# Performance work log

Hardware: AMD Instinct MI355X
Metric: run time of the kernel (lower is better)

The kernel has to match this reference:

```python
import jax, jax.numpy as jnp
import numpy as np

D_MODEL = 1024
N_HEADS = 16
D_K = D_MODEL // N_HEADS
THETA = 10000.0
B, S = 4, 2048


def setup_inputs() -> dict:
    key = jax.random.key(0)
    ks = jax.random.split(key, 5)
    scale = 0.02
    return {
        "x": jax.random.normal(ks[0], (B, S, D_MODEL), dtype=jnp.float32),
        "token_positions": jnp.arange(S, dtype=jnp.int32),
        "WQ": jax.random.normal(ks[1], (D_MODEL, D_MODEL), dtype=jnp.float32) * scale,
        "WK": jax.random.normal(ks[2], (D_MODEL, D_MODEL), dtype=jnp.float32) * scale,
        "WV": jax.random.normal(ks[3], (D_MODEL, D_MODEL), dtype=jnp.float32) * scale,
        "WO": jax.random.normal(ks[4], (D_MODEL, D_MODEL), dtype=jnp.float32) * scale,
    }


def apply_rope(x, positions):
    # x: [B, H, S, d_k]; rotate interleaved (even, odd) pairs
    half = D_K // 2
    inv_freq = THETA ** (-jnp.arange(half, dtype=x.dtype) * 2.0 / D_K)  # [half]
    ang = positions.astype(x.dtype)[:, None] * inv_freq[None, :]        # [S, half]
    cos, sin = jnp.cos(ang), jnp.sin(ang)
    x1 = x[..., 0::2]
    x2 = x[..., 1::2]
    r1 = x1 * cos - x2 * sin
    r2 = x1 * sin + x2 * cos
    return jnp.stack([r1, r2], axis=-1).reshape(x.shape)


def reference(x, token_positions, WQ, WK, WV, WO):
    b, s, _ = x.shape
    # Linear (no bias), weight stored (out, in): y = x @ W^T
    def proj(W):
        y = jnp.einsum('bsd,ed->bse', x, W)
        return y.reshape(b, s, N_HEADS, D_K).transpose(0, 2, 1, 3)  # [b,h,s,dk]
    Q, K, V = proj(WQ), proj(WK), proj(WV)
    Q = apply_rope(Q, token_positions)
    K = apply_rope(K, token_positions)
    scores = jnp.einsum('bhqd,bhkd->bhqk', Q, K) / jnp.sqrt(jnp.asarray(D_K, x.dtype))
    causal = jnp.tril(jnp.ones((s, s), dtype=bool))
    scores = jnp.where(causal, scores, -jnp.inf)
    attn = jax.nn.softmax(scores, axis=-1)
    out = jnp.einsum('bhqk,bhkd->bhqd', attn, V)
    out = out.transpose(0, 2, 1, 3).reshape(b, s, D_MODEL)
    return jnp.einsum('bse,de->bsd', out, WO)
```

## Files before the change

### kernel.cpp

```cpp
#include <hip/hip_runtime.h>
#include <cstdint>
#include <cstddef>

#define DM 1024
#define NH 16
#define DKD 64
#define BB 4
#define SS 2048
#define MTOT (BB*SS)

typedef float  f32x4  __attribute__((ext_vector_type(4)));
typedef __bf16 bf16x8 __attribute__((ext_vector_type(8)));
typedef __bf16 bf16x4v __attribute__((ext_vector_type(4)));
typedef __bf16 bf16x2v __attribute__((ext_vector_type(2)));
using as3v = __attribute__((address_space(3))) void;
using as1v = __attribute__((address_space(1))) void;

__device__ __forceinline__ void gl2lds16(const void* g, void* l) {
  __builtin_amdgcn_global_load_lds((as1v*)g, (as3v*)l, 16, 0, 0);
}

__device__ __forceinline__ float fast_exp2(float x) {
#if __has_builtin(__builtin_amdgcn_exp2f)
  return __builtin_amdgcn_exp2f(x);
#else
  return __expf(x * 0.6931471805599453f);
#endif
}

__device__ __forceinline__ void sincos_rev(float rev, float* s, float* c) {
#if __has_builtin(__builtin_amdgcn_sinf) && __has_builtin(__builtin_amdgcn_cosf)
  *s = __builtin_amdgcn_sinf(rev);
  *c = __builtin_amdgcn_cosf(rev);
#else
  float a = rev * 6.283185307179586f;
  *s = __sinf(a); *c = __cosf(a);
#endif
}

__device__ __forceinline__ uint32_t pkbf(float a, float b) {
  union { uint32_t u; __bf16 h[2]; } c;
  c.h[0] = (__bf16)a; c.h[1] = (__bf16)b;
  return c.u;
}

__global__ void cast_all_k(const float* __restrict__ x,
                           const float* __restrict__ wq, const float* __restrict__ wk,
                           const float* __restrict__ wv, const float* __restrict__ wo,
                           __bf16* __restrict__ xb,
                           __bf16* __restrict__ wqb, __bf16* __restrict__ wkb,
                           __bf16* __restrict__ wvb, __bf16* __restrict__ wob) {
  int i = blockIdx.x * blockDim.x + threadIdx.x;
  const float* src;
  __bf16* dst;
  int idx, oidx;
  if (i < 2097152) {
    src = x; dst = xb; idx = i; oidx = i;
  } else {
    int j = i - 2097152;
    int w = j >> 18;
    idx = j & 262143;
    src = (w == 0) ? wq : (w == 1) ? wk : (w == 2) ? wv : wo;
    dst = (w == 0) ? wqb : (w == 1) ? wkb : (w == 2) ? wvb : wob;
    if (w < 2) {
      int e = idx >> 8;
      int c = idx & 255;
      int d = e & 63;
      int dp = (d & 1) ? 32 + (d >> 1) : (d >> 1);
      oidx = (((e & ~63) | dp) << 8) | c;
    } else {
      oidx = idx;
    }
  }
  float4 f = ((const float4*)src)[idx];
  bf16x4v o;
  o[0] = (__bf16)f.x; o[1] = (__bf16)f.y; o[2] = (__bf16)f.z; o[3] = (__bf16)f.w;
  ((bf16x4v*)dst)[oidx] = o;
}

__global__ void rope_tbl_k(const int* __restrict__ pos, float2* __restrict__ tbl) {
  int p = blockIdx.x * blockDim.x + threadIdx.x;
  int s = p >> 5;
  int i = p & 31;
  float ps = (float)pos[s];
  float invr = __expf(-0.28782313663f * (float)i) * 0.15915494309f;
  float rev = ps * invr;
  rev -= floorf(rev);
  float sn, cs;
  sincos_rev(rev, &sn, &cs);
  tbl[p] = make_float2(cs, sn);
}


template <typename CT>
__global__ __launch_bounds__(256, 4) void gemm_bt_k(const __bf16* __restrict__ A,
                                                    const __bf16* __restrict__ B,
                                                    CT* __restrict__ C,
                                                    int M, int N, int K) {
  __shared__ __bf16 As[2][128 * 32];
  __shared__ __bf16 Bs[2][128 * 32];
  const int tid  = threadIdx.x;
  const int lane = tid & 63;
  const int wid  = tid >> 6;
  const int lrow = lane & 15;
  const int quad = lane >> 4;
  const int m0 = blockIdx.y * 128;
  const int n0 = blockIdx.x * 128;
  const int wm = (wid & 1) * 64;
  const int wn = (wid >> 1) * 64;

  const int r0 = wid * 32 + (lane >> 2);
  const int cs = (((r0 & 1) << 2) | (lane & 3)) ^ ((r0 >> 1) & 7);
  const int gr = (r0 & ~1) | (cs >> 2);
  const int gc = cs & 3;
  const __bf16* Asrc = A + (size_t)(m0 + gr) * K + gc * 8;
  const __bf16* Bsrc = B + (size_t)(n0 + gr) * K + gc * 8;
  const int clf = (((lrow & 1) << 2) + quad) ^ (lrow >> 1);

  f32x4 acc[4][4] = {};

  auto stage = [&](int buf, int k0) {
    gl2lds16(Asrc + k0,                   &As[buf][(wid * 32)      * 32]);
    gl2lds16(Asrc + (size_t)16 * K + k0,  &As[buf][(wid * 32 + 16) * 32]);
    gl2lds16(Bsrc + k0,                   &Bs[buf][(wid * 32)      * 32]);
    gl2lds16(Bsrc + (size_t)16 * K + k0,  &Bs[buf][(wid * 32 + 16) * 32]);
  };

  stage(0, 0);
  const int kiters = K >> 5;
  for (int kk = 0; kk < kiters; ++kk) {
    __syncthreads();
    if (kk + 1 < kiters) stage((kk + 1) & 1, (kk + 1) * 32);
    const __bf16* as = As[kk & 1];
    const __bf16* bs = Bs[kk & 1];

    bf16x8 af[4], bfr[4];
#pragma unroll
    for (int i = 0; i < 4; ++i)
      af[i] = *(const bf16x8*)(as + ((wm + i * 16 + lrow) >> 1) * 64 + clf * 8);
#pragma unroll
    for (int i = 0; i < 4; ++i)
      bfr[i] = *(const bf16x8*)(bs + ((wn + i * 16 + lrow) >> 1) * 64 + clf * 8);
    __builtin_amdgcn_s_setprio(1);
#pragma unroll
    for (int mi = 0; mi < 4; ++mi)
#pragma unroll
      for (int ni = 0; ni < 4; ++ni)
        acc[mi][ni] = __builtin_amdgcn_mfma_f32_16x16x32_bf16(af[mi], bfr[ni], acc[mi][ni], 0, 0, 0);
    __builtin_amdgcn_s_setprio(0);
  }

#pragma unroll
  for (int mi = 0; mi < 4; ++mi)
#pragma unroll
    for (int ni = 0; ni < 4; ++ni)
#pragma unroll
      for (int r = 0; r < 4; ++r) {
        int row = m0 + wm + mi * 16 + quad * 4 + r;
        int col = n0 + wn + ni * 16 + lrow;
        C[(size_t)row * N + col] = (CT)acc[mi][ni][r];
      }
}

__global__ __launch_bounds__(256, 4) void gemm_qkv_k(const __bf16* __restrict__ A,
                                                     const __bf16* __restrict__ Bq,
                                                     const __bf16* __restrict__ Bk,
                                                     const __bf16* __restrict__ Bv,
                                                     const float2* __restrict__ tbl,
                                                     __bf16* __restrict__ Cq,
                                                     __bf16* __restrict__ Ck,
                                                     __bf16* __restrict__ Cv) {
  __shared__ __bf16 As[2][128 * 32];
  __shared__ __bf16 Bs[2][128 * 32];
  const int sel = blockIdx.x >> 3;
  const __bf16* B = sel == 0 ? Bq : sel == 1 ? Bk : Bv;
  const int n0 = (blockIdx.x & 7) * 128;
  const int m0 = blockIdx.y * 128;
  const int K = DM;
  const int tid  = threadIdx.x;
  const int lane = tid & 63;
  const int wid  = tid >> 6;
  const int lrow = lane & 15;
  const int quad = lane >> 4;
  const int wm = (wid & 1) * 64;
  const int wn = (wid >> 1) * 64;

  const int r0 = wid * 32 + (lane >> 2);
  const int cs = (((r0 & 1) << 2) | (lane & 3)) ^ ((r0 >> 1) & 7);
  const int gr = (r0 & ~1) | (cs >> 2);
  const int gc = cs & 3;
  const __bf16* Asrc = A + (size_t)(m0 + gr) * K + gc * 8;
  const __bf16* Bsrc = B + (size_t)(n0 + gr) * K + gc * 8;
  const int clf = (((lrow & 1) << 2) + quad) ^ (lrow >> 1);

  f32x4 acc[4][4] = {};

  auto stage = [&](int buf, int k0) {
    gl2lds16(Asrc + k0,                   &As[buf][(wid * 32)      * 32]);
    gl2lds16(Asrc + (size_t)16 * K + k0,  &As[buf][(wid * 32 + 16) * 32]);
    gl2lds16(Bsrc + k0,                   &Bs[buf][(wid * 32)      * 32]);
    gl2lds16(Bsrc + (size_t)16 * K + k0,  &Bs[buf][(wid * 32 + 16) * 32]);
  };

  stage(0, 0);
  const int kiters = K >> 5;
  for (int kk = 0; kk < kiters; ++kk) {
    __syncthreads();
    if (kk + 1 < kiters) stage((kk + 1) & 1, (kk + 1) * 32);
    const __bf16* as = As[kk & 1];
    const __bf16* bs = Bs[kk & 1];

    bf16x8 af[4], bfr[4];
#pragma unroll
    for (int i = 0; i < 4; ++i)
      af[i] = *(const bf16x8*)(as + ((wm + i * 16 + lrow) >> 1) * 64 + clf * 8);
#pragma unroll
    for (int i = 0; i < 4; ++i)
      bfr[i] = *(const bf16x8*)(bs + ((wn + i * 16 + lrow) >> 1) * 64 + clf * 8);
    __builtin_amdgcn_s_setprio(1);
#pragma unroll
    for (int mi = 0; mi < 4; ++mi)
#pragma unroll
      for (int ni = 0; ni < 4; ++ni)
        acc[mi][ni] = __builtin_amdgcn_mfma_f32_16x16x32_bf16(af[mi], bfr[ni], acc[mi][ni], 0, 0, 0);
    __builtin_amdgcn_s_setprio(0);
  }

  const int hbase = (n0 + wn) >> 6;
  const int bq = m0 >> 11;

  if (sel == 2) {
    __bf16* vt = Cv + ((size_t)(bq * NH + hbase)) * (DKD * SS);
    const int S0 = (m0 + wm) & (SS - 1);
#pragma unroll
    for (int ni = 0; ni < 4; ++ni) {
      const int d = ni * 16 + lrow;
#pragma unroll
      for (int mi = 0; mi < 4; ++mi) {
        bf16x4v pk;
#pragma unroll
        for (int r = 0; r < 4; ++r) pk[r] = (__bf16)acc[mi][ni][r];
        const int sp = S0 + (mi >> 1) * 32 + quad * 8 + (mi & 1) * 4;
        *(bf16x4v*)(vt + (size_t)d * SS + sp) = pk;
      }
    }
  } else {
    __bf16* C = ((sel == 0) ? Cq : Ck) + ((size_t)(bq * NH + hbase)) * (SS * DKD);
#pragma unroll
    for (int ni = 0; ni < 2; ++ni) {
      const int i = ni * 16 + lrow;
#pragma unroll
      for (int mi = 0; mi < 4; ++mi) {
#pragma unroll
        for (int r = 0; r < 4; ++r) {
          int s = (m0 + wm + mi * 16 + quad * 4 + r) & (SS - 1);
          float2 cssn = tbl[s * 32 + i];
          float a = acc[mi][ni][r];
          float b = acc[mi][ni + 2][r];
          C[(size_t)s * DKD + i]      = (__bf16)fmaf(a, cssn.x, -(b * cssn.y));
          C[(size_t)s * DKD + 32 + i] = (__bf16)fmaf(a, cssn.y,  (b * cssn.x));
        }
      }
    }
  }
}

__global__ __launch_bounds__(512, 4) void attn10_k(const __bf16* __restrict__ Qh,
                                                   const __bf16* __restrict__ Kh,
                                                   const __bf16* __restrict__ VT,
                                                   __bf16* __restrict__ O) {
  __shared__ __bf16 Ks[2][128 * 64];
  __shared__ __bf16 Vt[2][64 * 128];
  const int tid  = threadIdx.x;
  const int lane = tid & 63;
  const int wid  = tid >> 6;
  const int lrow = lane & 15;
  const int quad = lane >> 4;
  const int j   = blockIdx.x;
  const int xcd = j & 7;
  const int t   = j >> 3;
  const int bh  = (xcd << 3) | (t >> 3);
  const int pr  = t & 7;
  const int qa  = pr;
  const int qb  = 15 - pr;
  const int na  = qa + 1;
  const int b  = bh >> 4;
  const int h  = bh & 15;
  const size_t hb = (size_t)bh * (SS * DKD);

  const int skr = lane >> 3;
  const int skc = lane & 7;
  const int svd = lane >> 4;
  const int svc = lane & 15;

  auto stage = [&](int kt, int bsel) {
#pragma unroll
    for (int ii = 0; ii < 2; ++ii) {
      int i = wid * 2 + ii;
      int key = i * 8 + skr;
      int gc = skc ^ (key & 7);
      gl2lds16(Kh + hb + (size_t)(kt * 128 + key) * DKD + gc * 8, &Ks[bsel][i * 512]);
      int dk = i * 4 + svd;
      int gc2 = (svc & 8) | ((svc ^ dk) & 7);
      gl2lds16(VT + hb + (size_t)dk * SS + kt * 128 + gc2 * 8, &Vt[bsel][i * 512]);
    }
  };

  stage(0, 0);
  int it = 0;

  for (int seg = 0; seg < 2; ++seg) {
    const int qi  = seg ? qb : qa;
    const int q0  = qi * 128;
    const int nkt = qi + 1;
    const int qg  = q0 + wid * 16 + lrow;

    bf16x8 qf0, qf1;
    {
      const __bf16* qp = Qh + hb + (size_t)qg * DKD + quad * 8;
      qf0 = *(const bf16x8*)qp;
      qf1 = *(const bf16x8*)(qp + 32);
    }
    f32x4 Oa[4] = {};
    float la = 0.f, lb = 0.f;

    for (int kt = 0; kt < nkt; ++kt, ++it) {
      __syncthreads();
      {
        int nit = it + 1;
        if (nit < 17) {
          int nk = (nit < na) ? nit : (nit - na);
          stage(nk, nit & 1);
        }
      }
      const __bf16* ks = Ks[it & 1];
      const __bf16* vt = Vt[it & 1];

      f32x4 sa[8];
#pragma unroll
      for (int mi = 0; mi < 8; ++mi) sa[mi] = (f32x4){0.f, 0.f, 0.f, 0.f};
      __builtin_amdgcn_s_setprio(1);
#pragma unroll
      for (int tt = 0; tt < 2; ++tt) {
        bf16x8 qf = tt ? qf1 : qf0;
#pragma unroll
        for (int mi = 0; mi < 8; ++mi) {
          bf16x8 kf = *(const bf16x8*)(ks + (mi * 16 + lrow) * 64 + (((tt * 4 + quad) ^ (lrow & 7)) * 8));
          sa[mi] = __builtin_amdgcn_mfma_f32_16x16x32_bf16(kf, qf, sa[mi], 0, 0, 0);
        }
      }
      __builtin_amdgcn_s_setprio(0);

      const bool lastt = (kt == nkt - 1);
#pragma unroll
      for (int kc = 0; kc < 4; ++kc) {
        union { uint32_t u[4]; bf16x8 v; } P;
#pragma unroll
        for (int half = 0; half < 2; ++half) {
          const int mi = kc * 2 + half;
          float pr4[4];
#pragma unroll
          for (int r = 0; r < 4; ++r) {
            float p = fast_exp2(sa[mi][r] * 0.18033688f - 8.0f);
            if (lastt) {
              int key = kt * 128 + kc * 32 + half * 16 + quad * 4 + r;
              p = (key <= qg) ? p : 0.f;
            }
            pr4[r] = p;
          }
          float s01 = pr4[0] + pr4[1];
          float s23 = pr4[2] + pr4[3];
          if (half) lb += (s01 + s23); else la += (s01 + s23);
          P.u[half * 2]     = pkbf(pr4[0], pr4[1]);
          P.u[half * 2 + 1] = pkbf(pr4[2], pr4[3]);
        }
        __builtin_amdgcn_s_setprio(1);
#pragma unroll
        for (int ni = 0; ni < 4; ++ni) {
          int c = kc * 4 + quad;
          int cp = (c & 8) | ((c ^ (lrow & 7)) & 7);
          bf16x8 vf = *(const bf16x8*)(vt + (ni * 16 + lrow) * 128 + cp * 8);
          Oa[ni] = __builtin_amdgcn_mfma_f32_16x16x32_bf16(P.v, vf, Oa[ni], 0, 0, 0);
        }
        __builtin_amdgcn_s_setprio(0);
      }
    }

    float l = la + lb;
    l += __shfl_xor(l, 16, 64);
    l += __shfl_xor(l, 32, 64);
#pragma unroll
    for (int r = 0; r < 4; ++r) {
      float li = __shfl(l, quad * 4 + r, 64);
      float inv = 1.0f / li;
      int row = q0 + wid * 16 + quad * 4 + r;
#pragma unroll
      for (int ni = 0; ni < 4; ++ni)
        O[(size_t)b * SS * DM + (size_t)row * DM + h * DKD + ni * 16 + lrow] =
            (__bf16)(Oa[ni][r] * inv);
    }
  }
}

extern "C" void kernel_launch(void* const* d_in, const int* in_sizes, int n_in,
                              void* d_out, int out_size, void* d_ws, size_t ws_size,
                              hipStream_t stream) {
  (void)in_sizes; (void)n_in; (void)out_size; (void)ws_size;
  const float* x  = (const float*)d_in[0];
  const int*   pos = (const int*)d_in[1];
  const float* WQ = (const float*)d_in[2];
  const float* WK = (const float*)d_in[3];
  const float* WV = (const float*)d_in[4];
  const float* WO = (const float*)d_in[5];
  float* out = (float*)d_out;

  char* w = (char*)d_ws;
  const size_t MB = 1024 * 1024;
  __bf16* xb  = (__bf16*)(w);
  __bf16* wqb = (__bf16*)(w + 16 * MB);
  __bf16* wkb = (__bf16*)(w + 18 * MB);
  __bf16* wvb = (__bf16*)(w + 20 * MB);
  __bf16* wob = (__bf16*)(w + 22 * MB);
  __bf16* Qh  = (__bf16*)(w + 24 * MB);
  __bf16* Kh  = (__bf16*)(w + 40 * MB);
  __bf16* Cb  = (__bf16*)(w + 56 * MB);
  __bf16* VT  = (__bf16*)(w + 72 * MB);
  float2* tbl = (float2*)(w + 88 * MB);

  cast_all_k<<<3145728 / 256, 256, 0, stream>>>(x, WQ, WK, WV, WO, xb, wqb, wkb, wvb, wob);

  rope_tbl_k<<<(SS * 32) / 256, 256, 0, stream>>>(pos, tbl);

  gemm_qkv_k<<<dim3(24, MTOT / 128), 256, 0, stream>>>(xb, wqb, wkb, wvb, tbl, Qh, Kh, VT);

  attn10_k<<<dim3(512), 512, 0, stream>>>(Qh, Kh, VT, Cb);

  gemm_bt_k<float><<<dim3(DM / 128, MTOT / 128), 256, 0, stream>>>(Cb, wob, out, MTOT, DM, DM);
}
```

Baseline: 260.5 us.

## Deepen GEMM LDS pipeline to four stages with explicit vmcnt waits

Both the generic GEMM and the fused QKV GEMM go from a double-buffered LDS pipeline with __syncthreads to a 4-buffer ring that prefetches three k-tiles ahead. Fine-grained s_waitcnt vmcnt counts and raw s_barrier calls replace the full sync, so more global loads stay in flight behind the MFMAs. This doubles LDS use per block to 64KB and lowers launch bounds occupancy from 4 to 2 blocks per CU. Hand-counted vmcnt values carry a correctness risk if the compiler emits other vector memory ops.

After: 250.5 us. 1.04x faster.

```diff
diff --git a/kernel.cpp b/kernel.cpp
--- a/kernel.cpp
+++ b/kernel.cpp
@@ -19,6 +19,10 @@
 __device__ __forceinline__ void gl2lds16(const void* g, void* l) {
   __builtin_amdgcn_global_load_lds((as1v*)g, (as3v*)l, 16, 0, 0);
 }
+
+#define BAR() asm volatile("s_barrier" ::: "memory")
+#define WAITV(NSTR) asm volatile("s_waitcnt vmcnt(" NSTR ")" ::: "memory")
+#define SCHEDB() __builtin_amdgcn_sched_barrier(0)
 
 __device__ __forceinline__ float fast_exp2(float x) {
 #if __has_builtin(__builtin_amdgcn_exp2f)
@@ -93,12 +97,12 @@
 
 
 template <typename CT>
-__global__ __launch_bounds__(256, 4) void gemm_bt_k(const __bf16* __restrict__ A,
+__global__ __launch_bounds__(256, 2) void gemm_bt_k(const __bf16* __restrict__ A,
                                                     const __bf16* __restrict__ B,
                                                     CT* __restrict__ C,
                                                     int M, int N, int K) {
-  __shared__ __bf16 As[2][128 * 32];
-  __shared__ __bf16 Bs[2][128 * 32];
+  __shared__ __bf16 As[4][128 * 32];
+  __shared__ __bf16 Bs[4][128 * 32];
   const int tid  = threadIdx.x;
   const int lane = tid & 63;
   const int wid  = tid >> 6;
@@ -119,21 +123,19 @@
 
   f32x4 acc[4][4] = {};
 
-  auto stage = [&](int buf, int k0) {
+  auto stage = [&](int kt) {
+    const int buf = kt & 3;
+    const int k0 = kt * 32;
     gl2lds16(Asrc + k0,                   &As[buf][(wid * 32)      * 32]);
     gl2lds16(Asrc + (size_t)16 * K + k0,  &As[buf][(wid * 32 + 16) * 32]);
     gl2lds16(Bsrc + k0,                   &Bs[buf][(wid * 32)      * 32]);
     gl2lds16(Bsrc + (size_t)16 * K + k0,  &Bs[buf][(wid * 32 + 16) * 32]);
   };
 
-  stage(0, 0);
-  const int kiters = K >> 5;
-  for (int kk = 0; kk < kiters; ++kk) {
-    __syncthreads();
-    if (kk + 1 < kiters) stage((kk + 1) & 1, (kk + 1) * 32);
-    const __bf16* as = As[kk & 1];
-    const __bf16* bs = Bs[kk & 1];
-
+  auto kstep = [&](int kt, bool dostage) {
+    if (dostage) stage(kt + 3);
+    const __bf16* as = As[kt & 3];
+    const __bf16* bs = Bs[kt & 3];
     bf16x8 af[4], bfr[4];
 #pragma unroll
     for (int i = 0; i < 4; ++i)
@@ -148,7 +150,18 @@
       for (int ni = 0; ni < 4; ++ni)
         acc[mi][ni] = __builtin_amdgcn_mfma_f32_16x16x32_bf16(af[mi], bfr[ni], acc[mi][ni], 0, 0, 0);
     __builtin_amdgcn_s_setprio(0);
+  };
+
+  const int kiters = K >> 5;
+  stage(0); stage(1); stage(2);
+  WAITV("8"); BAR(); SCHEDB();
+  for (int kt = 0; kt < kiters - 3; ++kt) {
+    kstep(kt, true);
+    WAITV("8"); BAR(); SCHEDB();
   }
+  kstep(kiters - 3, false); WAITV("4"); BAR(); SCHEDB();
+  kstep(kiters - 2, false); WAITV("0"); BAR(); SCHEDB();
+  kstep(kiters - 1, false);
 
 #pragma unroll
   for (int mi = 0; mi < 4; ++mi)
@@ -162,7 +175,7 @@
       }
 }
 
-__global__ __launch_bounds__(256, 4) void gemm_qkv_k(const __bf16* __restrict__ A,
+__global__ __launch_bounds__(256, 2) void gemm_qkv_k(const __bf16* __restrict__ A,
                                                      const __bf16* __restrict__ Bq,
                                                      const __bf16* __restrict__ Bk,
                                                      const __bf16* __restrict__ Bv,
@@ -170,8 +183,8 @@
                                                      __bf16* __restrict__ Cq,
                                                      __bf16* __restrict__ Ck,
                                                      __bf16* __restrict__ Cv) {
-  __shared__ __bf16 As[2][128 * 32];
-  __shared__ __bf16 Bs[2][128 * 32];
+  __shared__ __bf16 As[4][128 * 32];
+  __shared__ __bf16 Bs[4][128 * 32];
   const int sel = blockIdx.x >> 3;
   const __bf16* B = sel == 0 ? Bq : sel == 1 ? Bk : Bv;
   const int n0 = (blockIdx.x & 7) * 128;
@@ -195,21 +208,19 @@
 
   f32x4 acc[4][4] = {};
 
-  auto stage = [&](int buf, int k0) {
+  auto stage = [&](int kt) {
+    const int buf = kt & 3;
+    const int k0 = kt * 32;
     gl2lds16(Asrc + k0,                   &As[buf][(wid * 32)      * 32]);
     gl2lds16(Asrc + (size_t)16 * K + k0,  &As[buf][(wid * 32 + 16) * 32]);
     gl2lds16(Bsrc + k0,                   &Bs[buf][(wid * 32)      * 32]);
     gl2lds16(Bsrc + (size_t)16 * K + k0,  &Bs[buf][(wid * 32 + 16) * 32]);
   };
 
-  stage(0, 0);
-  const int kiters = K >> 5;
-  for (int kk = 0; kk < kiters; ++kk) {
-    __syncthreads();
-    if (kk + 1 < kiters) stage((kk + 1) & 1, (kk + 1) * 32);
-    const __bf16* as = As[kk & 1];
-    const __bf16* bs = Bs[kk & 1];
-
+  auto kstep = [&](int kt, bool dostage) {
+    if (dostage) stage(kt + 3);
+    const __bf16* as = As[kt & 3];
+    const __bf16* bs = Bs[kt & 3];
     bf16x8 af[4], bfr[4];
 #pragma unroll
     for (int i = 0; i < 4; ++i)
@@ -224,7 +235,18 @@
       for (int ni = 0; ni < 4; ++ni)
         acc[mi][ni] = __builtin_amdgcn_mfma_f32_16x16x32_bf16(af[mi], bfr[ni], acc[mi][ni], 0, 0, 0);
     __builtin_amdgcn_s_setprio(0);
+  };
+
+  const int kiters = K >> 5;
+  stage(0); stage(1); stage(2);
+  WAITV("8"); BAR(); SCHEDB();
+  for (int kt = 0; kt < kiters - 3; ++kt) {
+    kstep(kt, true);
+    WAITV("8"); BAR(); SCHEDB();
   }
+  kstep(kiters - 3, false); WAITV("4"); BAR(); SCHEDB();
+  kstep(kiters - 2, false); WAITV("0"); BAR(); SCHEDB();
+  kstep(kiters - 1, false);
 
   const int hbase = (n0 + wn) >> 6;
   const int bq = m0 >> 11;
```
